# Kernel optimization log

Measured on AMD Instinct MI355X. Metric: run time of the kernel, lower is better.

Reference implementation:

```python
import jax, jax.numpy as jnp
import numpy as np


def setup_inputs() -> dict:
    key = jax.random.key(0)
    B, N = 256, 512
    # binary symmetric-ish adjacency (0/1 entries)
    adj = jax.random.randint(key, (B, N, N), 0, 2).astype(jnp.float32)
    return {"adjacency": adj}


def reference(adjacency):
    # atom mask: rows with any connection
    atom_mask = (jnp.sum(adjacency, axis=-1) != 0).astype(adjacency.dtype)  # [B, N]
    N = adjacency.shape[-1]
    eye = jnp.eye(N, dtype=adjacency.dtype)
    # set_diag(adjacency, atom_mask): zero existing diagonal, insert mask
    adjacency_hat = adjacency * (1.0 - eye) + eye * atom_mask[..., :, None]
    degree_hat = jnp.sum(adjacency_hat, axis=-1)  # [B, N]
    d_sqrt = jnp.sqrt(degree_hat)
    # reciprocal_no_nan: 1/x where x != 0, else 0
    d_inv_sqrt = jnp.where(d_sqrt == 0, 0.0, 1.0 / jnp.where(d_sqrt == 0, 1.0, d_sqrt))
    # D^-1/2 A_hat D^-1/2 as row/column scaling (equivalent to the diag matmuls)
    adjacency_norm = d_inv_sqrt[..., :, None] * adjacency_hat * d_inv_sqrt[..., None, :]
    return adjacency_norm
```

## Files before the change

kernel.cpp:

```cpp
#include <hip/hip_runtime.h>
#include <hip/hip_bf16.h>


#define NCOL 512
#define NB   256

__global__ __launch_bounds__(256) void degree_kernel(
    const float* __restrict__ adj, float* __restrict__ dinv, int totalRows) {
    int gtid = blockIdx.x * blockDim.x + threadIdx.x;
    int row  = gtid >> 6;
    int lane = threadIdx.x & 63;
    if (row >= totalRows) return;

    const float4* r4 = (const float4*)(adj + (size_t)row * NCOL);
    float4 a0 = r4[lane];
    float4 a1 = r4[lane + 64];

    float s = (a0.x + a0.y) + (a0.z + a0.w) + (a1.x + a1.y) + (a1.z + a1.w);

    int i = row & (NCOL - 1);
    float diag = 0.0f;
    int j0 = lane << 2;
    if (i >= j0 && i < j0 + 4) {
        const float* p = (const float*)&a0;
        diag = p[i - j0];
    }
    int j1 = 256 + (lane << 2);
    if (i >= j1 && i < j1 + 4) {
        const float* p = (const float*)&a1;
        diag = p[i - j1];
    }

    #pragma unroll
    for (int off = 32; off > 0; off >>= 1) {
        s    += __shfl_xor(s, off);
        diag += __shfl_xor(diag, off);
    }

    if (lane == 0) {
        float mask = (s != 0.0f) ? 1.0f : 0.0f;
        float deg  = s - diag + mask;
        dinv[row]  = (deg > 0.0f) ? (1.0f / sqrtf(deg)) : 0.0f;
    }
}

__global__ __launch_bounds__(256) void scale_kernel(
    const float* __restrict__ adj, const float* __restrict__ dinv,
    float* __restrict__ out) {
    size_t idx4 = (size_t)blockIdx.x * blockDim.x + threadIdx.x;
    int    j4   = (int)(idx4 & 127);
    size_t row  = idx4 >> 7;
    int    i    = (int)(row & (NCOL - 1));
    size_t rowb = row & ~(size_t)(NCOL - 1);

    float4 a  = ((const float4*)adj)[idx4];
    float4 dj = ((const float4*)(dinv + rowb))[j4];
    float  di = dinv[row];

    int j = j4 << 2;
    float4 o;
    o.x = (di * ((j + 0 == i) ? 1.0f : a.x)) * dj.x;
    o.y = (di * ((j + 1 == i) ? 1.0f : a.y)) * dj.y;
    o.z = (di * ((j + 2 == i) ? 1.0f : a.z)) * dj.z;
    o.w = (di * ((j + 3 == i) ? 1.0f : a.w)) * dj.w;

    ((float4*)out)[idx4] = o;
}

extern "C" void kernel_launch(void* const* d_in, const int* in_sizes, int n_in,
                              void* d_out, int out_size, void* d_ws, size_t ws_size,
                              hipStream_t stream) {
    const float* adj = (const float*)d_in[0];
    float* out  = (float*)d_out;
    float* dinv = (float*)d_ws;

    const int totalRows = NB * NCOL;

    degree_kernel<<<totalRows / 4, 256, 0, stream>>>(adj, dinv, totalRows);

    const size_t total4 = (size_t)NB * NCOL * NCOL / 4;
    scale_kernel<<<(unsigned)(total4 / 256), 256, 0, stream>>>(adj, dinv, out);
}
```

Before: 471.5 us.

## Fuse degree and scaling into one per-batch kernel with shared dinv

Replaces the two kernels with a single kernel that handles one batch matrix per 1024-thread block. The block first computes the inverse sqrt degrees into shared memory, then rescales the matrix, iterating rows in reverse so recently read data is more likely still in cache, and writes output with nontemporal stores. This removes the separate dinv round trip and a launch, and aims to get the second read of the adjacency from cache. The cost is only 256 blocks, so occupancy and latency hiding are limited.

```diff
diff --git a/kernel.cpp b/kernel.cpp
--- a/kernel.cpp
+++ b/kernel.cpp
@@ -2,82 +2,74 @@
 #include <hip/hip_bf16.h>
 
 
-#define NCOL 512
-#define NB   256
+#define NN 512
+#define NB 256
 
-__global__ __launch_bounds__(256) void degree_kernel(
-    const float* __restrict__ adj, float* __restrict__ dinv, int totalRows) {
-    int gtid = blockIdx.x * blockDim.x + threadIdx.x;
-    int row  = gtid >> 6;
-    int lane = threadIdx.x & 63;
-    if (row >= totalRows) return;
+typedef float f32x4 __attribute__((ext_vector_type(4)));
 
-    const float4* r4 = (const float4*)(adj + (size_t)row * NCOL);
-    float4 a0 = r4[lane];
-    float4 a1 = r4[lane + 64];
+__global__ __launch_bounds__(1024) void fused_norm_kernel(
+    const float* __restrict__ adj, float* __restrict__ out) {
+    __shared__ float sdinv[NN];
 
-    float s = (a0.x + a0.y) + (a0.z + a0.w) + (a1.x + a1.y) + (a1.z + a1.w);
+    const int b = blockIdx.x;
+    const size_t base4 = (size_t)b * (NN * (NN / 4));
+    const f32x4* a4 = (const f32x4*)adj + base4;
+    f32x4*       o4 = (f32x4*)out + base4;
 
-    int i = row & (NCOL - 1);
-    float diag = 0.0f;
-    int j0 = lane << 2;
-    if (i >= j0 && i < j0 + 4) {
-        const float* p = (const float*)&a0;
-        diag = p[i - j0];
+    const int tid  = threadIdx.x;
+    const int wave = tid >> 6;
+    const int lane = tid & 63;
+
+    for (int rr = 0; rr < 32; ++rr) {
+        const int row = wave * 32 + rr;
+        const f32x4* r4 = a4 + row * (NN / 4);
+        f32x4 x0 = r4[lane];
+        f32x4 x1 = r4[lane + 64];
+
+        float s = (x0.x + x0.y) + (x0.z + x0.w) + (x1.x + x1.y) + (x1.z + x1.w);
+
+        float diag = 0.0f;
+        int j0 = lane << 2;
+        if (row >= j0 && row < j0 + 4) diag = ((const float*)&x0)[row - j0];
+        int j1 = 256 + (lane << 2);
+        if (row >= j1 && row < j1 + 4) diag = ((const float*)&x1)[row - j1];
+
+        #pragma unroll
+        for (int off = 32; off > 0; off >>= 1) {
+            s    += __shfl_xor(s, off);
+            diag += __shfl_xor(diag, off);
+        }
+        if (lane == 0) {
+            float mask = (s != 0.0f) ? 1.0f : 0.0f;
+            float deg  = s - diag + mask;
+            sdinv[row] = (deg > 0.0f) ? (1.0f / sqrtf(deg)) : 0.0f;
+        }
     }
-    int j1 = 256 + (lane << 2);
-    if (i >= j1 && i < j1 + 4) {
-        const float* p = (const float*)&a1;
-        diag = p[i - j1];
+    __syncthreads();
+
+    const int j4    = tid & 127;
+    const int rbase = tid >> 7;
+    const f32x4 dj = ((const f32x4*)sdinv)[j4];
+    const int jj = j4 << 2;
+
+    for (int it = 63; it >= 0; --it) {
+        const int row = rbase + (it << 3);
+        const float di = sdinv[row];
+        const size_t k = (size_t)row * (NN / 4) + j4;
+        f32x4 a = a4[k];
+        f32x4 o;
+        o.x = (di * ((jj + 0 == row) ? 1.0f : a.x)) * dj.x;
+        o.y = (di * ((jj + 1 == row) ? 1.0f : a.y)) * dj.y;
+        o.z = (di * ((jj + 2 == row) ? 1.0f : a.z)) * dj.z;
+        o.w = (di * ((jj + 3 == row) ? 1.0f : a.w)) * dj.w;
+        __builtin_nontemporal_store(o, &o4[k]);
     }
-
-    #pragma unroll
-    for (int off = 32; off > 0; off >>= 1) {
-        s    += __shfl_xor(s, off);
-        diag += __shfl_xor(diag, off);
-    }
-
-    if (lane == 0) {
-        float mask = (s != 0.0f) ? 1.0f : 0.0f;
-        float deg  = s - diag + mask;
-        dinv[row]  = (deg > 0.0f) ? (1.0f / sqrtf(deg)) : 0.0f;
-    }
-}
-
-__global__ __launch_bounds__(256) void scale_kernel(
-    const float* __restrict__ adj, const float* __restrict__ dinv,
-    float* __restrict__ out) {
-    size_t idx4 = (size_t)blockIdx.x * blockDim.x + threadIdx.x;
-    int    j4   = (int)(idx4 & 127);
-    size_t row  = idx4 >> 7;
-    int    i    = (int)(row & (NCOL - 1));
-    size_t rowb = row & ~(size_t)(NCOL - 1);
-
-    float4 a  = ((const float4*)adj)[idx4];
-    float4 dj = ((const float4*)(dinv + rowb))[j4];
-    float  di = dinv[row];
-
-    int j = j4 << 2;
-    float4 o;
-    o.x = (di * ((j + 0 == i) ? 1.0f : a.x)) * dj.x;
-    o.y = (di * ((j + 1 == i) ? 1.0f : a.y)) * dj.y;
-    o.z = (di * ((j + 2 == i) ? 1.0f : a.z)) * dj.z;
-    o.w = (di * ((j + 3 == i) ? 1.0f : a.w)) * dj.w;
-
-    ((float4*)out)[idx4] = o;
 }
 
 extern "C" void kernel_launch(void* const* d_in, const int* in_sizes, int n_in,
                               void* d_out, int out_size, void* d_ws, size_t ws_size,
                               hipStream_t stream) {
     const float* adj = (const float*)d_in[0];
-    float* out  = (float*)d_out;
-    float* dinv = (float*)d_ws;
-
-    const int totalRows = NB * NCOL;
-
-    degree_kernel<<<totalRows / 4, 256, 0, stream>>>(adj, dinv, totalRows);
-
-    const size_t total4 = (size_t)NB * NCOL * NCOL / 4;
-    scale_kernel<<<(unsigned)(total4 / 256), 256, 0, stream>>>(adj, dinv, out);
+    float* out = (float*)d_out;
+    fused_norm_kernel<<<NB, 1024, 0, stream>>>(adj, out);
 }
```

After: 484.8 us. 2.8% more time.
